# Optimization experiments

Hardware: AMD Instinct MI355X
Metric: run time of the kernel (lower is better)

## Reference

```python
import jax, jax.numpy as jnp
import numpy as np

NUM_LAYERS = 2
SHAPES = [(100, 100), (50, 50), (25, 25), (13, 13)]  # (H, W) per level
D, NH, NP, NL = 256, 8, 4, 4
DH = D // NH
DFF = 1024
B = 2
S = sum(h * w for h, w in SHAPES)  # 13294


def layer_norm(x, g, b, eps=1e-5):
    m = x.mean(-1, keepdims=True)
    v = jnp.var(x, axis=-1, keepdims=True)
    return (x - m) * jax.lax.rsqrt(v + eps) * g + b


def get_reference_points(valid_ratios):
    refs = []
    for lvl, (H_, W_) in enumerate(SHAPES):
        ry, rx = jnp.meshgrid(jnp.linspace(0.5, H_ - 0.5, H_),
                              jnp.linspace(0.5, W_ - 0.5, W_), indexing='ij')
        ry = ry.reshape(-1)[None] / (valid_ratios[:, None, lvl, 1] * H_)
        rx = rx.reshape(-1)[None] / (valid_ratios[:, None, lvl, 0] * W_)
        refs.append(jnp.stack([rx, ry], -1))
    ref = jnp.concatenate(refs, 1)                      # [B, S, 2]
    return ref[:, :, None] * valid_ratios[:, None]      # [B, S, NL, 2]


def sample_level(value_l, H_, W_, loc):
    # value_l: [B, nH, H*W, Dh]; loc: [B, Q, nH, P, 2] normalized in [0,1]
    x = loc[..., 0] * W_ - 0.5
    y = loc[..., 1] * H_ - 0.5
    x0 = jnp.floor(x)
    y0 = jnp.floor(y)
    Bq, Q = loc.shape[0], loc.shape[1]
    acc = 0.
    corners = ((x0, y0, (x0 + 1 - x) * (y0 + 1 - y)),
               (x0 + 1, y0, (x - x0) * (y0 + 1 - y)),
               (x0, y0 + 1, (x0 + 1 - x) * (y - y0)),
               (x0 + 1, y0 + 1, (x - x0) * (y - y0)))
    for xi, yi, w in corners:  # zero-padding grid_sample: invalid corners contribute 0
        valid = (xi >= 0) & (xi <= W_ - 1) & (yi >= 0) & (yi <= H_ - 1)
        idx = (jnp.clip(yi, 0, H_ - 1) * W_ + jnp.clip(xi, 0, W_ - 1)).astype(jnp.int32)
        idx = jnp.transpose(idx, (0, 2, 1, 3)).reshape(Bq, NH, Q * NP)
        g = jnp.take_along_axis(value_l, idx[..., None], axis=2)  # [B,nH,Q*P,Dh]
        wv = jnp.transpose((w * valid).astype(value_l.dtype), (0, 2, 1, 3)).reshape(Bq, NH, Q * NP)
        acc = acc + g * wv[..., None]
    return acc.reshape(Bq, NH, Q, NP, DH)


def msda(query, ref, src, W_val, b_val, W_off, b_off, W_attn, b_attn, W_out, b_out):
    Bq, Q = query.shape[:2]
    value = (src @ W_val + b_val).reshape(Bq, S, NH, DH)
    off = (query @ W_off + b_off).reshape(Bq, Q, NH, NL, NP, 2)
    attn = jax.nn.softmax((query @ W_attn + b_attn).reshape(Bq, Q, NH, NL * NP), -1)
    attn = attn.reshape(Bq, Q, NH, NL, NP)
    normalizer = jnp.array([[w, h] for h, w in SHAPES], dtype=query.dtype)  # [NL,2] (x,y)
    loc = ref[:, :, None, :, None, :] + off / normalizer[None, None, None, :, None, :]
    out = jnp.zeros((Bq, NH, Q, DH), query.dtype)
    start = 0
    for l, (H_, W_) in enumerate(SHAPES):
        v_l = jnp.transpose(value[:, start:start + H_ * W_], (0, 2, 1, 3))  # [B,nH,HW,Dh]
        samp = sample_level(v_l, H_, W_, loc[:, :, :, l])                    # [B,nH,Q,P,Dh]
        w_l = jnp.transpose(attn[:, :, :, l], (0, 2, 1, 3))                  # [B,nH,Q,P]
        out = out + (samp * w_l[..., None]).sum(3)
        start += H_ * W_
    out = jnp.transpose(out, (0, 2, 1, 3)).reshape(Bq, Q, D)
    return out @ W_out + b_out


def setup_inputs() -> dict:
    key = jax.random.key(0)
    ks = jax.random.split(key, 12)
    sc = 0.02
    inp = {
        'src': jax.random.normal(ks[0], (B, S, D), jnp.float32),
        'spatial_shapes': np.array(SHAPES, dtype=np.int64),
        'valid_ratios': jnp.ones((B, NL, 2), jnp.float32),
        'W_off': sc * jax.random.normal(ks[1], (NUM_LAYERS, D, NH * NL * NP * 2), jnp.float32),
        'b_off': jnp.zeros((NUM_LAYERS, NH * NL * NP * 2), jnp.float32),
        'W_attn': sc * jax.random.normal(ks[2], (NUM_LAYERS, D, NH * NL * NP), jnp.float32),
        'b_attn': jnp.zeros((NUM_LAYERS, NH * NL * NP), jnp.float32),
        'W_val': sc * jax.random.normal(ks[3], (NUM_LAYERS, D, D), jnp.float32),
        'b_val': jnp.zeros((NUM_LAYERS, D), jnp.float32),
        'W_out': sc * jax.random.normal(ks[4], (NUM_LAYERS, D, D), jnp.float32),
        'b_out': jnp.zeros((NUM_LAYERS, D), jnp.float32),
        'ln1_g': jnp.ones((NUM_LAYERS, D), jnp.float32),
        'ln1_b': jnp.zeros((NUM_LAYERS, D), jnp.float32),
        'W1': sc * jax.random.normal(ks[5], (NUM_LAYERS, D, DFF), jnp.float32),
        'b1': jnp.zeros((NUM_LAYERS, DFF), jnp.float32),
        'W2': sc * jax.random.normal(ks[6], (NUM_LAYERS, DFF, D), jnp.float32),
        'b2': jnp.zeros((NUM_LAYERS, D), jnp.float32),
        'ln2_g': jnp.ones((NUM_LAYERS, D), jnp.float32),
        'ln2_b': jnp.zeros((NUM_LAYERS, D), jnp.float32),
    }
    return inp


def reference(src, spatial_shapes, valid_ratios, W_off, b_off, W_attn, b_attn,
              W_val, b_val, W_out, b_out, ln1_g, ln1_b, W1, b1, W2, b2, ln2_g, ln2_b):
    # Deformable-DETR encoder stack (dropout=0 / eval mode, pos=None, no padding mask).
    ref = get_reference_points(valid_ratios)  # [B, S, NL, 2]
    x = src
    for i in range(NUM_LAYERS):
        x2 = msda(x, ref, x, W_val[i], b_val[i], W_off[i], b_off[i],
                  W_attn[i], b_attn[i], W_out[i], b_out[i])
        x = layer_norm(x + x2, ln1_g[i], ln1_b[i])
        h = jax.nn.relu(x @ W1[i] + b1[i]) @ W2[i] + b2[i]
        x = layer_norm(x + h, ln2_g[i], ln2_b[i])
    return x
```

## Files before the change

### kernel.cpp

```cpp
#include <hip/hip_runtime.h>
#include <math.h>


#define S_TOT 13294
#define BATCH 2
#define M_TOT (BATCH * S_TOT)
#define M_PAD 26624

typedef __attribute__((ext_vector_type(8))) short short8;
typedef __attribute__((ext_vector_type(4))) float floatx4;
typedef __attribute__((ext_vector_type(2))) float floatx2;

#define AS1C(p) ((const __attribute__((address_space(1))) void*)(p))
#define AS3(p)  ((__attribute__((address_space(3))) void*)(p))

static __device__ __forceinline__ unsigned short f2bf(float x) {
    union { float f; unsigned u; } v; v.f = x;
    unsigned r = v.u + 0x7FFFu + ((v.u >> 16) & 1u);
    return (unsigned short)(r >> 16);
}
static __device__ __forceinline__ float b2f(unsigned short u) {
    union { unsigned u; float f; } v; v.u = (unsigned)u << 16; return v.f;
}
static __device__ __forceinline__ float bflo(unsigned u) {
    union { unsigned u; float f; } v; v.u = u << 16; return v.f;
}
static __device__ __forceinline__ float bfhi(unsigned u) {
    union { unsigned u; float f; } v; v.u = u & 0xFFFF0000u; return v.f;
}
static __device__ __forceinline__ float braw(unsigned u) {
    union { unsigned u; float f; } v; v.u = u; return v.f;
}

template<int TM, bool RELU, bool BF16OUT, bool PROJ, bool SUM>
__global__ __launch_bounds__(256)
void mgemm(const unsigned short* __restrict__ A,
           const unsigned short* __restrict__ BT,
           const float* __restrict__ bias,
           const float* __restrict__ bias2,
           const float* __restrict__ bias3,
           const unsigned short* __restrict__ R,
           unsigned short* __restrict__ Cb,
           unsigned short* __restrict__ Cb2,
           int nbmPer,
           int M, int N, int K)
{
    constexpr int WM = (TM == 128) ? 2 : 1;
    constexpr int WN = 4 / WM;
    constexpr int MI = TM / (WM * 16);
    constexpr int NI = 128 / (WN * 16);
    __shared__ __align__(16) unsigned short smemA[2 * TM * 32];
    __shared__ __align__(16) unsigned short smemB[2 * 128 * 32];
    const int tid  = threadIdx.x;
    const int lane = tid & 63;
    const int w    = tid >> 6;
    const int wm   = w % WM, wn = w / WM;
    const int lr   = lane & 15, quad = lane >> 4;
    const int id  = blockIdx.x;
    const int x8  = id & 7;
    const int k9  = id >> 3;
    const int bm  = (x8 * nbmPer + (k9 % nbmPer)) * TM;
    const int bn  = (k9 / nbmPer) * 128;

    floatx4 acc[MI][NI];
    #pragma unroll
    for (int i = 0; i < MI; ++i)
        #pragma unroll
        for (int j = 0; j < NI; ++j)
            acc[i][j] = (floatx4){0.f, 0.f, 0.f, 0.f};

    const int srow = lane >> 2;
    const int selt = (lane & 3) << 3;

    for (int k0 = 0; k0 < K; k0 += 64) {
        #pragma unroll
        for (int c = 0; c < 2; ++c) {
            if (TM == 128) {
                #pragma unroll
                for (int jj = 0; jj < 2; ++jj) {
                    const int j = 2 * w + jj;
                    const unsigned short* ga = A  + (size_t)(bm + j * 16 + srow) * K + k0 + c * 32 + selt;
                    const unsigned short* gb = BT + (size_t)(bn + j * 16 + srow) * K + k0 + c * 32 + selt;
                    __builtin_amdgcn_global_load_lds(AS1C(ga), AS3(smemA + c * (TM * 32) + j * 512), 16, 0, 0);
                    __builtin_amdgcn_global_load_lds(AS1C(gb), AS3(smemB + c * 4096 + j * 512), 16, 0, 0);
                }
            } else {
                const unsigned short* ga = A + (size_t)(bm + w * 16 + srow) * K + k0 + c * 32 + selt;
                __builtin_amdgcn_global_load_lds(AS1C(ga), AS3(smemA + c * (TM * 32) + w * 512), 16, 0, 0);
                #pragma unroll
                for (int jj = 0; jj < 2; ++jj) {
                    const int j = 2 * w + jj;
                    const unsigned short* gb = BT + (size_t)(bn + j * 16 + srow) * K + k0 + c * 32 + selt;
                    __builtin_amdgcn_global_load_lds(AS1C(gb), AS3(smemB + c * 4096 + j * 512), 16, 0, 0);
                }
            }
        }
        __syncthreads();

        #pragma unroll
        for (int c = 0; c < 2; ++c) {
            short8 av[MI], bv[NI];
            #pragma unroll
            for (int mi = 0; mi < MI; ++mi)
                av[mi] = *(const short8*)&smemA[c * (TM * 32) + (wm * MI * 16 + mi * 16 + lr) * 32 + quad * 8];
            #pragma unroll
            for (int ni = 0; ni < NI; ++ni)
                bv[ni] = *(const short8*)&smemB[c * 4096 + (wn * NI * 16 + ni * 16 + lr) * 32 + quad * 8];
            #pragma unroll
            for (int mi = 0; mi < MI; ++mi)
                #pragma unroll
                for (int ni = 0; ni < NI; ++ni)
                    acc[mi][ni] = __builtin_amdgcn_mfma_f32_16x16x32_bf16(
                        av[mi], bv[ni], acc[mi][ni], 0, 0, 0);
        }
        __syncthreads();
    }

    #pragma unroll
    for (int mi = 0; mi < MI; ++mi) {
        #pragma unroll
        for (int ni = 0; ni < NI; ++ni) {
            #pragma unroll
            for (int r = 0; r < 4; ++r) {
                const int row = bm + wm * MI * 16 + mi * 16 + quad * 4 + r;
                const int col = bn + wn * NI * 16 + ni * 16 + lr;
                if (PROJ) {
                    const float bb = (col < 256) ? bias[col]
                                   : (col < 512) ? bias2[col - 256]
                                                 : bias3[col - 512];
                    const float v = acc[mi][ni][r] + bb;
                    if (col < 256) Cb[(size_t)row * 256 + col] = f2bf(v);
                    else           Cb2[(size_t)row * 384 + (col - 256)] = f2bf(v);
                } else if (SUM) {
                    const float v = acc[mi][ni][r] + bias[col]
                                  + b2f(R[(size_t)row * 256 + col]);
                    Cb[(size_t)row * 256 + col] = f2bf(v);
                } else {
                    float v = acc[mi][ni][r] + bias[col];
                    if (RELU) v = fmaxf(v, 0.0f);
                    if (BF16OUT) Cb[(size_t)row * N + col] = f2bf(v);
                }
            }
        }
    }
}

template<bool HASF, bool HASB>
__global__ __launch_bounds__(256)
void ln_kernel(const unsigned short* __restrict__ S,
               const float* __restrict__ g, const float* __restrict__ beta,
               float* __restrict__ outF, unsigned short* __restrict__ outB,
               int M)
{
    const int half = (threadIdx.x & 63) >> 5;
    const int l32  = threadIdx.x & 31;
    const int row  = blockIdx.x * 8 + (threadIdx.x >> 6) * 2 + half;
    if (row >= M) return;
    const int c8 = l32 * 8;
    const uint4 sv = *(const uint4*)(S + (size_t)row * 256 + c8);
    float x[8];
    x[0] = bflo(sv.x); x[1] = bfhi(sv.x);
    x[2] = bflo(sv.y); x[3] = bfhi(sv.y);
    x[4] = bflo(sv.z); x[5] = bfhi(sv.z);
    x[6] = bflo(sv.w); x[7] = bfhi(sv.w);
    float p = 0.f, q = 0.f;
    #pragma unroll
    for (int i = 0; i < 8; ++i) { p += x[i]; q += x[i] * x[i]; }
    #pragma unroll
    for (int o = 1; o < 32; o <<= 1) {
        p += __shfl_xor(p, o, 64);
        q += __shfl_xor(q, o, 64);
    }
    const float mean = p * (1.0f / 256.0f);
    const float var  = q * (1.0f / 256.0f) - mean * mean;
    const float rs   = rsqrtf(var + 1e-5f);
    const float4 gv0 = *(const float4*)(g + c8);
    const float4 gv1 = *(const float4*)(g + c8 + 4);
    const float4 bv0 = *(const float4*)(beta + c8);
    const float4 bv1 = *(const float4*)(beta + c8 + 4);
    const float gg[8] = {gv0.x, gv0.y, gv0.z, gv0.w, gv1.x, gv1.y, gv1.z, gv1.w};
    const float bb[8] = {bv0.x, bv0.y, bv0.z, bv0.w, bv1.x, bv1.y, bv1.z, bv1.w};
    float y[8];
    #pragma unroll
    for (int i = 0; i < 8; ++i)
        y[i] = (x[i] - mean) * rs * gg[i] + bb[i];
    if (HASF) {
        float4 o0; o0.x = y[0]; o0.y = y[1]; o0.z = y[2]; o0.w = y[3];
        float4 o1; o1.x = y[4]; o1.y = y[5]; o1.z = y[6]; o1.w = y[7];
        *(float4*)(outF + (size_t)row * 256 + c8) = o0;
        *(float4*)(outF + (size_t)row * 256 + c8 + 4) = o1;
    }
    if (HASB) {
        uint4 o2;
        o2.x = (unsigned)f2bf(y[0]) | ((unsigned)f2bf(y[1]) << 16);
        o2.y = (unsigned)f2bf(y[2]) | ((unsigned)f2bf(y[3]) << 16);
        o2.z = (unsigned)f2bf(y[4]) | ((unsigned)f2bf(y[5]) << 16);
        o2.w = (unsigned)f2bf(y[6]) | ((unsigned)f2bf(y[7]) << 16);
        *(uint4*)(outB + (size_t)row * 256 + c8) = o2;
    }
}

__global__ __launch_bounds__(256)
void convpad(const float* __restrict__ X, unsigned short* __restrict__ Y, int M)
{
    const int idx = blockIdx.x * 256 + threadIdx.x;
    const int row = idx >> 6;
    const int c4  = (idx & 63) << 2;
    if (row >= M_PAD) return;
    float4 v = {0.f, 0.f, 0.f, 0.f};
    if (row < M) v = ((const float4*)(X + (size_t)row * 256))[c4 >> 2];
    unsigned p0 = (unsigned)f2bf(v.x) | ((unsigned)f2bf(v.y) << 16);
    unsigned p1 = (unsigned)f2bf(v.z) | ((unsigned)f2bf(v.w) << 16);
    uint2 o; o.x = p0; o.y = p1;
    *(uint2*)(Y + (size_t)row * 256 + c4) = o;
}

struct WJobs {
    const float* W[12];
    unsigned short* WT[12];
    int K[12], N[12], tx[12], start[12];
};

__global__ __launch_bounds__(256)
void wtrans_all(WJobs jb)
{
    __shared__ float t[32][33];
    const int bx = blockIdx.x;
    int seg = 0;
    #pragma unroll
    for (int s = 1; s < 12; ++s) if (bx >= jb.start[s]) seg = s;
    const float* W = jb.W[seg];
    unsigned short* WT = jb.WT[seg];
    const int K = jb.K[seg], N = jb.N[seg], tx = jb.tx[seg];
    const int local = bx - jb.start[seg];
    const int n0 = (local % tx) * 32, k0 = (local / tx) * 32;
    const int c = threadIdx.x & 31, r0 = threadIdx.x >> 5;
    #pragma unroll
    for (int rr = r0; rr < 32; rr += 8)
        t[rr][c] = W[(size_t)(k0 + rr) * N + n0 + c];
    __syncthreads();
    #pragma unroll
    for (int rr = r0; rr < 32; rr += 8)
        WT[(size_t)(n0 + rr) * K + k0 + c] = f2bf(t[c][rr]);
}

__global__ __launch_bounds__(256)
void msda_kernel(const unsigned short* __restrict__ valb,
                 const unsigned short* __restrict__ oab,
                 const float* __restrict__ vr,
                 unsigned short* __restrict__ out)
{
    __shared__ __align__(16) char smeta[8 * 128 * 32];
    const int t = threadIdx.x;
    const int bid = (blockIdx.x & 7) * 416 + (blockIdx.x >> 3);

    {
        const int wv = t >> 6, lane = t & 63;
        const int lqA = wv * 2 + (lane >> 5);
        const int bq = bid * 8 + lqA;
        const int h = (lane >> 2) & 7;
        const int j = lane & 3;
        if (bq < M_TOT) {
            const int b = (bq >= S_TOT) ? 1 : 0;
            const int q = bq - b * S_TOT;
            const int bofs = b * (S_TOT * 512);
            int Hq, rr, cc, lq;
            if (q < 10000)      { lq = 0; Hq = 100; rr = q / 100;              cc = q - rr * 100; }
            else if (q < 12500) { lq = 1; Hq = 50;  int r2 = q - 10000; rr = r2 / 50; cc = r2 - rr * 50; }
            else if (q < 13125) { lq = 2; Hq = 25;  int r2 = q - 12500; rr = r2 / 25; cc = r2 - rr * 25; }
            else                { lq = 3; Hq = 13;  int r2 = q - 13125; rr = r2 / 13; cc = r2 - rr * 13; }
            const float rxb = (cc + 0.5f) / (vr[(b * 4 + lq) * 2 + 0] * (float)Hq);
            const float ryb = (rr + 0.5f) / (vr[(b * 4 + lq) * 2 + 1] * (float)Hq);
            const int HWt[4] = {100, 50, 25, 13};
            const int stt[4] = {0, 10000, 12500, 13125};
            const int HW = HWt[j], st = stt[j];
            const float fW = (float)HW;
            const float refxw = rxb * vr[(b * 4 + j) * 2 + 0] * fW - 0.5f;
            const float refyw = ryb * vr[(b * 4 + j) * 2 + 1] * fW - 0.5f;
            const unsigned short* row = oab + (size_t)bq * 384;
            const uint2 lgu = *(const uint2*)(row + 256 + h * 16 + j * 4);
            const float l0 = bflo(lgu.x), l1 = bfhi(lgu.x);
            const float l2 = bflo(lgu.y), l3 = bfhi(lgu.y);
            float mx = fmaxf(fmaxf(l0, l1), fmaxf(l2, l3));
            mx = fmaxf(mx, __shfl_xor(mx, 1, 64));
            mx = fmaxf(mx, __shfl_xor(mx, 2, 64));
            const float e0 = __expf(l0 - mx), e1 = __expf(l1 - mx);
            const float e2 = __expf(l2 - mx), e3 = __expf(l3 - mx);
            float ss = e0 + e1 + e2 + e3;
            ss += __shfl_xor(ss, 1, 64);
            ss += __shfl_xor(ss, 2, 64);
            const float inv = 1.0f / ss;
            const uint4 ou = *(const uint4*)(row + h * 32 + j * 8);
            const float oxs[4] = {bflo(ou.x), bflo(ou.y), bflo(ou.z), bflo(ou.w)};
            const float oys[4] = {bfhi(ou.x), bfhi(ou.y), bfhi(ou.z), bfhi(ou.w)};
            const float aw[4]  = {e0 * inv, e1 * inv, e2 * inv, e3 * inv};
            char* mb = smeta + (size_t)(lqA * 128 + h * 16 + j * 4) * 32;
            const int swz = ((h * 4 + j) & 7) << 4;
            #pragma unroll
            for (int p = 0; p < 4; ++p) {
                const float x = refxw + oxs[p];
                const float y = refyw + oys[p];
                const float x0f = floorf(x), y0f = floorf(y);
                const int x0 = (int)x0f, y0 = (int)y0f;
                const float fx = x - x0f, fy = y - y0f;
                const float wb[4] = {(1.f - fx) * (1.f - fy), fx * (1.f - fy),
                                     (1.f - fx) * fy,         fx * fy};
                const int xs[2] = {x0, x0 + 1};
                const int ys2[2] = {y0, y0 + 1};
                int iv[4]; float wv4[4];
                #pragma unroll
                for (int k = 0; k < 4; ++k) {
                    const int xi = xs[k & 1], yi = ys2[k >> 1];
                    const bool vld = ((unsigned)xi < (unsigned)HW) && ((unsigned)yi < (unsigned)HW);
                    const int xc = min(max(xi, 0), HW - 1);
                    const int yc = min(max(yi, 0), HW - 1);
                    iv[k] = bofs + ((st + yc * HW + xc) << 9) + (h << 6);
                    wv4[k] = vld ? wb[k] * aw[p] : 0.0f;
                }
                int4 i4; i4.x = iv[0]; i4.y = iv[1]; i4.z = iv[2]; i4.w = iv[3];
                float4 w4; w4.x = wv4[0]; w4.y = wv4[1]; w4.z = wv4[2]; w4.w = wv4[3];
                *(int4*)(mb + ((p * 32) ^ swz)) = i4;
                *(float4*)(mb + ((p * 32 + 16) ^ swz)) = w4;
            }
        }
    }
    __syncthreads();
    {
        const int lq2 = t >> 5;
        const int r = t & 31;
        const int h2 = r >> 2;
        const int cg = r & 3;
        const int bq2 = bid * 8 + lq2;
        if (bq2 < M_TOT) {
            const char* vbase = (const char*)valb;
            const unsigned cgo = cg * 16;
            floatx2 a0 = {0.f, 0.f}, a1 = {0.f, 0.f}, a2 = {0.f, 0.f}, a3 = {0.f, 0.f};
            const char* mb2 = smeta + (size_t)(lq2 * 128 + h2 * 16) * 32;
            #pragma unroll 4
            for (int s = 0; s < 16; ++s) {
                const int swz2 = ((h2 * 4 + (s >> 2)) & 7) << 4;
                const int4  iv = *(const int4*)(mb2 + ((s * 32) ^ swz2));
                const float4 w4 = *(const float4*)(mb2 + ((s * 32 + 16) ^ swz2));
                const uint4 u0 = *(const uint4*)(vbase + (unsigned)(iv.x + cgo));
                const uint4 u1 = *(const uint4*)(vbase + (unsigned)(iv.y + cgo));
                const uint4 u2 = *(const uint4*)(vbase + (unsigned)(iv.z + cgo));
                const uint4 u3 = *(const uint4*)(vbase + (unsigned)(iv.w + cgo));
                #define ACC8(UU, WW) { \
                    const floatx2 w2 = {WW, WW}; \
                    const floatx2 t0 = {bflo(UU.x), braw(UU.x)}; \
                    const floatx2 t1 = {bflo(UU.y), braw(UU.y)}; \
                    const floatx2 t2 = {bflo(UU.z), braw(UU.z)}; \
                    const floatx2 t3 = {bflo(UU.w), braw(UU.w)}; \
                    a0 += w2 * t0; a1 += w2 * t1; a2 += w2 * t2; a3 += w2 * t3; }
                ACC8(u0, w4.x) ACC8(u1, w4.y) ACC8(u2, w4.z) ACC8(u3, w4.w)
                #undef ACC8
            }
            uint4 o;
            o.x = (unsigned)f2bf(a0.x) | ((unsigned)f2bf(a0.y) << 16);
            o.y = (unsigned)f2bf(a1.x) | ((unsigned)f2bf(a1.y) << 16);
            o.z = (unsigned)f2bf(a2.x) | ((unsigned)f2bf(a2.y) << 16);
            o.w = (unsigned)f2bf(a3.x) | ((unsigned)f2bf(a3.y) << 16);
            *(uint4*)(out + (size_t)bq2 * 256 + h2 * 32 + cg * 8) = o;
        }
    }
}

extern "C" void kernel_launch(void* const* d_in, const int* in_sizes, int n_in,
                              void* d_out, int out_size, void* d_ws, size_t ws_size,
                              hipStream_t stream)
{
    const float* src    = (const float*)d_in[0];
    const float* vr     = (const float*)d_in[2];
    const float* W_off  = (const float*)d_in[3];
    const float* b_off  = (const float*)d_in[4];
    const float* W_attn = (const float*)d_in[5];
    const float* b_attn = (const float*)d_in[6];
    const float* W_val  = (const float*)d_in[7];
    const float* b_val  = (const float*)d_in[8];
    const float* W_out  = (const float*)d_in[9];
    const float* b_out  = (const float*)d_in[10];
    const float* ln1_g  = (const float*)d_in[11];
    const float* ln1_b  = (const float*)d_in[12];
    const float* W1     = (const float*)d_in[13];
    const float* b1     = (const float*)d_in[14];
    const float* W2     = (const float*)d_in[15];
    const float* b2     = (const float*)d_in[16];
    const float* ln2_g  = (const float*)d_in[17];
    const float* ln2_b  = (const float*)d_in[18];
    float* out = (float*)d_out;

    const int M = M_TOT;

    char* wsb = (char*)d_ws;
    unsigned short* HBF  = (unsigned short*)wsb;
    unsigned short* OAB  = (unsigned short*)wsb;
    unsigned short* VALB = (unsigned short*)(wsb + 20447232);
    unsigned short* S1   = (unsigned short*)wsb;
    unsigned short* X1B  = (unsigned short*)(wsb + 54525952);
    unsigned short* S2   = (unsigned short*)(wsb + 68157440);
    unsigned short* RB   = (unsigned short*)(wsb + 81788928);
    unsigned short* YBF  = (unsigned short*)(wsb + 95420416);
    unsigned short* WT   = (unsigned short*)(wsb + 109051904);

    const size_t LWT = 753664;
    const size_t oProj = 0, oOut = 163840, oW1 = 229376, oW2 = 491520;

    WJobs jb;
    int startAcc = 0;
    for (int i = 0; i < 2; ++i) {
        unsigned short* wt = WT + i * LWT;
        const float* srcs[6] = {W_val + i * 65536, W_off + i * 65536, W_attn + i * 32768,
                                W_out + i * 65536, W1 + i * 262144, W2 + i * 262144};
        unsigned short* dsts[6] = {wt + oProj, wt + oProj + 65536, wt + oProj + 131072,
                                   wt + oOut, wt + oW1, wt + oW2};
        const int Ks[6] = {256, 256, 256, 256, 256, 1024};
        const int Ns[6] = {256, 256, 128, 256, 1024, 256};
        for (int s = 0; s < 6; ++s) {
            const int idx = i * 6 + s;
            jb.W[idx] = srcs[s]; jb.WT[idx] = dsts[s];
            jb.K[idx] = Ks[s]; jb.N[idx] = Ns[s]; jb.tx[idx] = Ns[s] / 32;
            jb.start[idx] = startAcc;
            startAcc += (Ns[s] / 32) * (Ks[s] / 32);
        }
    }
    wtrans_all<<<dim3(startAcc), 256, 0, stream>>>(jb);

    const int GM128 = M_PAD / 128;
    const int GM64  = M_PAD / 64;
    const int GLN   = (M_TOT + 7) / 8;
    const dim3 blk(256);

    for (int i = 0; i < 2; ++i) {
        unsigned short* wt = WT + i * LWT;

        if (i == 0)
            convpad<<<dim3(M_PAD / 4), blk, 0, stream>>>(src, RB, M);

        mgemm<64, false, false, true, false><<<dim3(5 * GM64), blk, 0, stream>>>(
            RB, wt + oProj, b_val + i * 256, b_off + i * 256, b_attn + i * 128,
            nullptr, VALB, OAB, GM64 / 8, M, 640, 256);

        msda_kernel<<<dim3(3328), blk, 0, stream>>>(VALB, OAB, vr, YBF);

        mgemm<64, false, false, false, true><<<dim3(2 * GM64), blk, 0, stream>>>(
            YBF, wt + oOut, b_out + i * 256, nullptr, nullptr,
            RB, S1, nullptr, GM64 / 8, M, 256, 256);

        ln_kernel<false, true><<<dim3(GLN), blk, 0, stream>>>(
            S1, ln1_g + i * 256, ln1_b + i * 256, nullptr, X1B, M);

        mgemm<128, true, true, false, false><<<dim3(8 * GM128), blk, 0, stream>>>(
            X1B, wt + oW1, b1 + i * 1024, nullptr, nullptr,
            nullptr, HBF, nullptr, GM128 / 8, M, 1024, 256);

        mgemm<64, false, false, false, true><<<dim3(2 * GM64), blk, 0, stream>>>(
            HBF, wt + oW2, b2 + i * 256, nullptr, nullptr,
            X1B, S2, nullptr, GM64 / 8, M, 256, 1024);

        if (i == 0)
            ln_kernel<false, true><<<dim3(GLN), blk, 0, stream>>>(
                S2, ln2_g + i * 256, ln2_b + i * 256, nullptr, RB, M);
        else
            ln_kernel<true, false><<<dim3(GLN), blk, 0, stream>>>(
                S2, ln2_g + i * 256, ln2_b + i * 256, out, nullptr, M);
    }
}
```

Measured before the change: 388.3 us.

## Fuse FFN up-projection, ReLU and down-projection into one kernel

Replaces the two FFN GEMM launches with a single kernel. Each 64-row block keeps its input tile in LDS and loops over 64-wide hidden chunks: it computes the ReLU hidden chunk into shared memory and immediately accumulates it against the matching W2 slice. The residual is then added from the LDS copy of the input. This removes the round trip of the 1024-wide hidden activation through global memory and one launch, but the new kernel has no double buffering, uses several barriers per chunk and about 72KB of LDS, so occupancy and latency hiding may suffer.

```diff
diff --git a/kernel.cpp b/kernel.cpp
--- a/kernel.cpp
+++ b/kernel.cpp
@@ -143,6 +143,120 @@
             }
         }
     }
+}
+
+__global__ __launch_bounds__(256)
+void ffn_fused(const unsigned short* __restrict__ X,
+               const unsigned short* __restrict__ W1T,
+               const float* __restrict__ b1,
+               const unsigned short* __restrict__ W2T,
+               const float* __restrict__ b2,
+               unsigned short* __restrict__ S2,
+               int nbmPer)
+{
+    __shared__ __align__(16) unsigned short xs[16384];
+    __shared__ __align__(16) unsigned short wbuf[16384];
+    __shared__ __align__(16) unsigned short hbuf[4096];
+    const int lane = threadIdx.x & 63;
+    const int w    = threadIdx.x >> 6;
+    const int lr   = lane & 15, quad = lane >> 4;
+    const int srow = lane >> 2;
+    const int selt = (lane & 3) << 3;
+    const int id   = blockIdx.x;
+    const int bm   = ((id & 7) * nbmPer + (id >> 3)) * 64;
+
+    #pragma unroll
+    for (int c = 0; c < 8; ++c) {
+        const unsigned short* gx = X + (size_t)(bm + w * 16 + srow) * 256 + c * 32 + selt;
+        __builtin_amdgcn_global_load_lds(AS1C(gx), AS3(xs + c * 2048 + w * 512), 16, 0, 0);
+    }
+
+    floatx4 acc2[4][4];
+    #pragma unroll
+    for (int i = 0; i < 4; ++i)
+        #pragma unroll
+        for (int j = 0; j < 4; ++j)
+            acc2[i][j] = (floatx4){0.f, 0.f, 0.f, 0.f};
+
+    for (int kc = 0; kc < 16; ++kc) {
+        #pragma unroll
+        for (int c = 0; c < 8; ++c) {
+            const unsigned short* g1 = W1T + (size_t)(kc * 64 + w * 16 + srow) * 256 + c * 32 + selt;
+            __builtin_amdgcn_global_load_lds(AS1C(g1), AS3(wbuf + c * 2048 + w * 512), 16, 0, 0);
+        }
+        asm volatile("s_waitcnt vmcnt(0)" ::: "memory");
+        __builtin_amdgcn_s_barrier();
+
+        floatx4 acc1[4];
+        #pragma unroll
+        for (int mi = 0; mi < 4; ++mi) acc1[mi] = (floatx4){0.f, 0.f, 0.f, 0.f};
+        #pragma unroll
+        for (int kk = 0; kk < 8; ++kk) {
+            const short8 bv = *(const short8*)&wbuf[kk * 2048 + (w * 16 + lr) * 32 + quad * 8];
+            #pragma unroll
+            for (int mi = 0; mi < 4; ++mi) {
+                const short8 av = *(const short8*)&xs[kk * 2048 + (mi * 16 + lr) * 32 + quad * 8];
+                acc1[mi] = __builtin_amdgcn_mfma_f32_16x16x32_bf16(av, bv, acc1[mi], 0, 0, 0);
+            }
+        }
+        const float b1v = b1[kc * 64 + w * 16 + lr];
+        {
+            const int hcol = w * 16 + lr;
+            const int hc   = (hcol >> 5) * 2048 + (hcol & 31);
+            #pragma unroll
+            for (int mi = 0; mi < 4; ++mi)
+                #pragma unroll
+                for (int r = 0; r < 4; ++r) {
+                    const int hrow = mi * 16 + quad * 4 + r;
+                    hbuf[hc + hrow * 32] = f2bf(fmaxf(acc1[mi][r] + b1v, 0.f));
+                }
+        }
+        asm volatile("s_waitcnt lgkmcnt(0)" ::: "memory");
+        __builtin_amdgcn_s_barrier();
+
+        #pragma unroll
+        for (int c = 0; c < 2; ++c)
+            #pragma unroll
+            for (int jj = 0; jj < 4; ++jj) {
+                const int j = w * 4 + jj;
+                const unsigned short* g2 = W2T + (size_t)(j * 16 + srow) * 1024 + kc * 64 + c * 32 + selt;
+                __builtin_amdgcn_global_load_lds(AS1C(g2), AS3(wbuf + c * 8192 + j * 512), 16, 0, 0);
+            }
+        asm volatile("s_waitcnt vmcnt(0)" ::: "memory");
+        __builtin_amdgcn_s_barrier();
+
+        #pragma unroll
+        for (int kk = 0; kk < 2; ++kk) {
+            short8 av2[4], bv2[4];
+            #pragma unroll
+            for (int mi = 0; mi < 4; ++mi)
+                av2[mi] = *(const short8*)&hbuf[kk * 2048 + (mi * 16 + lr) * 32 + quad * 8];
+            #pragma unroll
+            for (int ni = 0; ni < 4; ++ni)
+                bv2[ni] = *(const short8*)&wbuf[kk * 8192 + (w * 64 + ni * 16 + lr) * 32 + quad * 8];
+            #pragma unroll
+            for (int mi = 0; mi < 4; ++mi)
+                #pragma unroll
+                for (int ni = 0; ni < 4; ++ni)
+                    acc2[mi][ni] = __builtin_amdgcn_mfma_f32_16x16x32_bf16(
+                        av2[mi], bv2[ni], acc2[mi][ni], 0, 0, 0);
+        }
+        asm volatile("s_waitcnt lgkmcnt(0)" ::: "memory");
+        __builtin_amdgcn_s_barrier();
+    }
+
+    #pragma unroll
+    for (int mi = 0; mi < 4; ++mi)
+        #pragma unroll
+        for (int ni = 0; ni < 4; ++ni)
+            #pragma unroll
+            for (int r = 0; r < 4; ++r) {
+                const int row = mi * 16 + quad * 4 + r;
+                const int col = w * 64 + ni * 16 + lr;
+                const float resid = b2f(xs[(col >> 5) * 2048 + row * 32 + (col & 31)]);
+                const float v = acc2[mi][ni][r] + b2[col] + resid;
+                S2[(size_t)(bm + row) * 256 + col] = f2bf(v);
+            }
 }
 
 template<bool HASF, bool HASB>
@@ -305,12 +419,12 @@
                 const float fx = x - x0f, fy = y - y0f;
                 const float wb[4] = {(1.f - fx) * (1.f - fy), fx * (1.f - fy),
                                      (1.f - fx) * fy,         fx * fy};
-                const int xs[2] = {x0, x0 + 1};
+                const int xs2[2] = {x0, x0 + 1};
                 const int ys2[2] = {y0, y0 + 1};
                 int iv[4]; float wv4[4];
                 #pragma unroll
                 for (int k = 0; k < 4; ++k) {
-                    const int xi = xs[k & 1], yi = ys2[k >> 1];
+                    const int xi = xs2[k & 1], yi = ys2[k >> 1];
                     const bool vld = ((unsigned)xi < (unsigned)HW) && ((unsigned)yi < (unsigned)HW);
                     const int xc = min(max(xi, 0), HW - 1);
                     const int yc = min(max(yi, 0), HW - 1);
@@ -392,7 +506,6 @@
     const int M = M_TOT;
 
     char* wsb = (char*)d_ws;
-    unsigned short* HBF  = (unsigned short*)wsb;
     unsigned short* OAB  = (unsigned short*)wsb;
     unsigned short* VALB = (unsigned short*)(wsb + 20447232);
     unsigned short* S1   = (unsigned short*)wsb;
@@ -425,7 +538,6 @@
     }
     wtrans_all<<<dim3(startAcc), 256, 0, stream>>>(jb);
 
-    const int GM128 = M_PAD / 128;
     const int GM64  = M_PAD / 64;
     const int GLN   = (M_TOT + 7) / 8;
     const dim3 blk(256);
@@ -449,13 +561,9 @@
         ln_kernel<false, true><<<dim3(GLN), blk, 0, stream>>>(
             S1, ln1_g + i * 256, ln1_b + i * 256, nullptr, X1B, M);
 
-        mgemm<128, true, true, false, false><<<dim3(8 * GM128), blk, 0, stream>>>(
-            X1B, wt + oW1, b1 + i * 1024, nullptr, nullptr,
-            nullptr, HBF, nullptr, GM128 / 8, M, 1024, 256);
-
-        mgemm<64, false, false, false, true><<<dim3(2 * GM64), blk, 0, stream>>>(
-            HBF, wt + oW2, b2 + i * 256, nullptr, nullptr,
-            X1B, S2, nullptr, GM64 / 8, M, 256, 1024);
+        ffn_fused<<<dim3(GM64), blk, 0, stream>>>(
+            X1B, wt + oW1, b1 + i * 1024, wt + oW2, b2 + i * 256,
+            S2, GM64 / 8);
 
         if (i == 0)
             ln_kernel<false, true><<<dim3(GLN), blk, 0, stream>>>(
```

Result: faster. 376.7 us (-3.0%).
